# Kernel optimization log

Hardware: AMD Instinct MI355X
Metric: run time of the kernel (lower is better)

Reference implementation:

```python
import jax, jax.numpy as jnp
import numpy as np

N_NODES = 100000
N_EDGES = 1600000
D_FEAT = 256
HID = 128
DEG_DIM = 128  # data.degree_exist_matrix.shape[1]


def setup_inputs() -> dict:
    key = jax.random.key(0)
    ks = jax.random.split(key, 12)
    s = lambda fan_in: 1.0 / np.sqrt(fan_in)
    x = jax.random.normal(ks[0], (N_NODES, D_FEAT), dtype=jnp.float32)
    edge_index = jax.random.randint(ks[1], (2, N_EDGES), 0, N_NODES, dtype=jnp.int32)
    return {
        "x": x,
        "edge_index": edge_index,
        # GCNConv 1 / 2 (PyG stores weight [in,out], bias [out])
        "W1": jax.random.uniform(ks[2], (D_FEAT, HID), jnp.float32, -s(D_FEAT), s(D_FEAT)),
        "b1": jnp.zeros((HID,), jnp.float32),
        "W2": jax.random.uniform(ks[3], (HID, HID), jnp.float32, -s(HID), s(HID)),
        "b2": jnp.zeros((HID,), jnp.float32),
        # down_sample Linear(D_FEAT, HID)
        "Wd": jax.random.uniform(ks[4], (D_FEAT, HID), jnp.float32, -s(D_FEAT), s(D_FEAT)),
        "bd": jax.random.uniform(ks[5], (HID,), jnp.float32, -s(D_FEAT), s(D_FEAT)),
        # linear2: Degree_layer(HID, 1) ~ Linear(HID, 1)
        "Wdeg": jax.random.uniform(ks[6], (HID, 1), jnp.float32, -s(HID), s(HID)),
        "bdeg": jax.random.uniform(ks[7], (1,), jnp.float32, -s(HID), s(HID)),
        # linear3: Linear(HID, DEG_DIM)
        "W3": jax.random.uniform(ks[8], (HID, DEG_DIM), jnp.float32, -s(HID), s(HID)),
        "b3": jax.random.uniform(ks[9], (DEG_DIM,), jnp.float32, -s(HID), s(HID)),
    }


def gcn_conv(x, W, b, src, dst, n):
    """PyG GCNConv: D^-1/2 (A+I) D^-1/2 X W + b (symmetric norm, self-loops)."""
    h = x @ W  # [N, out]
    deg = jax.ops.segment_sum(jnp.ones_like(dst, dtype=h.dtype), dst, num_segments=n) + 1.0
    dinv = jax.lax.rsqrt(deg)  # deg >= 1 from self loop
    coef = dinv[src] * dinv[dst]  # [E]
    msgs = h[src] * coef[:, None]  # [E, out] -- dominant gather
    agg = jax.ops.segment_sum(msgs, dst, num_segments=n)
    agg = agg + h * (dinv * dinv)[:, None]  # self-loop contribution
    return agg + b


def reference(x, edge_index, W1, b1, W2, b2, Wd, bd, Wdeg, bdeg, W3, b3):
    n = x.shape[0]
    src, dst = edge_index[0], edge_index[1]
    original_x = x @ Wd + bd
    h = gcn_conv(x, W1, b1, src, dst, n)
    h = jax.nn.relu(h)  # dropout is identity in eval mode
    h = gcn_conv(h, W2, b2, src, dst, n)
    h = h + original_x  # residual
    result1 = jax.nn.log_softmax(h, axis=-1)        # [N, HID]
    result2 = (h @ Wdeg + bdeg).squeeze(-1)          # [N]
    result3 = h @ W3 + b3                            # [N, DEG_DIM]
    return (result1, result2, result3)
```

## Files before the change

### kernel.cpp

```cpp
#include <hip/hip_runtime.h>


typedef __attribute__((ext_vector_type(8))) short bf16x8;
typedef __attribute__((ext_vector_type(4))) float f32x4;

#define CDIV(a, b) (((a) + (b) - 1) / (b))

#define GLOBAL_AS __attribute__((address_space(1)))
#define LDS_AS __attribute__((address_space(3)))

__device__ __forceinline__ void gload16(const void* g, void* l) {
  __builtin_amdgcn_global_load_lds((const GLOBAL_AS unsigned int*)g,
                                   (LDS_AS unsigned int*)l, 16, 0, 0);
}

__device__ __forceinline__ float b2f(unsigned short u) {
  union { unsigned int i; float f; } x; x.i = ((unsigned int)u) << 16; return x.f;
}
__device__ __forceinline__ unsigned short f2b(float f) {
  union { float f; unsigned int i; } x; x.f = f;
  unsigned int r = x.i + 0x7fffu + ((x.i >> 16) & 1u);
  return (unsigned short)(r >> 16);
}
__device__ __forceinline__ void add2(float& a0, float& a1, unsigned int u) {
  union { unsigned int i; float f; } lo, hi;
  lo.i = u << 16; hi.i = u & 0xffff0000u;
  a0 += lo.f; a1 += hi.f;
}
__device__ __forceinline__ unsigned int pack2(float lo, float hi) {
  return __builtin_amdgcn_perm(__float_as_uint(hi) + 0x8000u,
                               __float_as_uint(lo) + 0x8000u, 0x07060302u);
}


__global__ void k_wtrans4(const float* __restrict__ W1, const float* __restrict__ Wd,
                          const float* __restrict__ W2, const float* __restrict__ W3,
                          unsigned short* __restrict__ W1t, unsigned short* __restrict__ Wdt,
                          unsigned short* __restrict__ W2t, unsigned short* __restrict__ W3t) {
  int idx = blockIdx.x * blockDim.x + threadIdx.x;
  const float* in; unsigned short* out; int K, N;
  if (idx < 32768)       { in = W1; out = W1t; K = 256; N = 128; }
  else if (idx < 65536)  { in = Wd; out = Wdt; K = 256; N = 128; idx -= 32768; }
  else if (idx < 81920)  { in = W2; out = W2t; K = 128; N = 128; idx -= 65536; }
  else if (idx < 98304)  { in = W3; out = W3t; K = 128; N = 128; idx -= 81920; }
  else return;
  int k = idx / N, n = idx - k * N;
  out[n * K + k] = f2b(in[idx]);
}

__global__ void k_scan1(const int* __restrict__ deg, int* __restrict__ lscan,
                        int* __restrict__ partials, float* __restrict__ dinv, int n) {
  __shared__ int sd[256];
  int tid = threadIdx.x;
  int base = blockIdx.x * 2048 + tid * 8;
  int v[8]; int tsum = 0;
#pragma unroll
  for (int i = 0; i < 8; ++i) {
    int idx = base + i;
    int xv = (idx < n) ? deg[idx] : 0;
    v[i] = xv; tsum += xv;
    if (idx < n) dinv[idx] = 1.0f / sqrtf((float)xv + 1.0f);
  }
  sd[tid] = tsum;
  __syncthreads();
  for (int off = 1; off < 256; off <<= 1) {
    int t = (tid >= off) ? sd[tid - off] : 0;
    __syncthreads();
    sd[tid] += t;
    __syncthreads();
  }
  int run = sd[tid] - tsum;
#pragma unroll
  for (int i = 0; i < 8; ++i) {
    int idx = base + i;
    if (idx < n) lscan[idx] = run;
    run += v[i];
  }
  if (tid == 255) partials[blockIdx.x] = sd[255];
}

__global__ void k_scan2(const int* __restrict__ partials, int* __restrict__ pprefix, int nb) {
  if (threadIdx.x == 0 && blockIdx.x == 0) {
    int run = 0;
    for (int i = 0; i < nb; ++i) { pprefix[i] = run; run += partials[i]; }
    pprefix[nb] = run;
  }
}

__global__ void k_scan3(const int* __restrict__ pprefix, int* row_start,
                        int* __restrict__ cursor, int n, int E) {
  int idx = blockIdx.x * blockDim.x + threadIdx.x;
  if (idx >= n) return;
  int v = row_start[idx] + pprefix[idx >> 11];
  row_start[idx] = v;
  cursor[idx] = v;
  if (idx == 0) row_start[n] = E;
}


#define BIN_CHUNK 4096
#define OVF_CAP 65536

__global__ __launch_bounds__(256) void k_binA(
    const int* __restrict__ ei, int E, int nbuck, int cap,
    int* __restrict__ deg, int2* __restrict__ pairs, int* __restrict__ bcnt,
    int2* __restrict__ ovf, int* __restrict__ ovf_cnt) {
  __shared__ int lcnt[256];
  __shared__ int lbase[256];
  int tid = threadIdx.x;
  for (int i = tid; i < nbuck; i += 256) lcnt[i] = 0;
  __syncthreads();
  int base_e = blockIdx.x * BIN_CHUNK;
  int src[16], dst[16], lofs[16];
#pragma unroll
  for (int i = 0; i < 16; ++i) {
    int e = base_e + i * 256 + tid;
    if (e < E) {
      int s = ei[e], d = ei[E + e];
      src[i] = s; dst[i] = d;
      atomicAdd(&deg[d], 1);
      lofs[i] = atomicAdd(&lcnt[d >> 9], 1);
    } else {
      dst[i] = -1;
    }
  }
  __syncthreads();
  for (int b = tid; b < nbuck; b += 256)
    lbase[b] = atomicAdd(&bcnt[b], lcnt[b]);
  __syncthreads();
#pragma unroll
  for (int i = 0; i < 16; ++i) {
    if (dst[i] < 0) continue;
    int b = dst[i] >> 9;
    int gpos = lbase[b] + lofs[i];
    if (gpos < cap) {
      pairs[(size_t)b * cap + gpos] = make_int2(src[i], dst[i]);
    } else {
      int op = atomicAdd(ovf_cnt, 1);
      if (op < OVF_CAP) ovf[op] = make_int2(src[i], dst[i]);
    }
  }
}

__global__ __launch_bounds__(256) void k_binB(
    const int2* __restrict__ pairs, const int* __restrict__ bcnt,
    int nbuck, int cap,
    const int2* __restrict__ ovf, const int* __restrict__ ovf_cnt,
    int* __restrict__ cursor, int* __restrict__ csr_src) {
  if ((int)blockIdx.x < nbuck) {
    int b = blockIdx.x;
    int cnt = bcnt[b]; if (cnt > cap) cnt = cap;
    const int2* p = pairs + (size_t)b * cap;
    for (int i = threadIdx.x; i < cnt; i += 256) {
      int2 e = p[i];
      int pos = atomicAdd(&cursor[e.y], 1);
      csr_src[pos] = e.x;
    }
  } else {
    int total = *ovf_cnt; if (total > OVF_CAP) total = OVF_CAP;
    int start = (blockIdx.x - nbuck) * 256 + threadIdx.x;
    for (int i = start; i < total; i += 8 * 256) {
      int2 e = ovf[i];
      int pos = atomicAdd(&cursor[e.y], 1);
      csr_src[pos] = e.x;
    }
  }
}


__global__ __launch_bounds__(512) void k_gemm_x2(
    const float* __restrict__ X,
    const unsigned short* __restrict__ B1t,
    const unsigned short* __restrict__ B2t,
    const float* __restrict__ bias2,
    const float* __restrict__ dinvp,
    unsigned short* __restrict__ O1, float* __restrict__ O2, int n) {
  __shared__ char lds[65536];
  const int flat = threadIdx.x;
  const int wave = flat >> 6, lane = flat & 63;
  const int l15 = lane & 15, q = lane >> 4;
  const int wM = wave >> 1, wN = wave & 1;
  const int rowBase = blockIdx.x * 128;
  const int colBase = wN * 64;

  auto stage = [&](int kb, int buf) {
    char* ldsA = lds + buf * 32768;
    char* ldsB = ldsA + 16384;
    const char* Xb = (const char*)X;
#pragma unroll
    for (int j = 0; j < 2; ++j) {
      int i = j * 512 + flat;
      int row = i >> 3, pslot = i & 7;
      int lslot = pslot ^ (row & 7);
      int rowc = rowBase + row; if (rowc >= n) rowc = n - 1;
      gload16(Xb + (size_t)rowc * 1024 + (size_t)(kb * 128 + lslot * 16),
              ldsA + (j * 512 + wave * 64) * 16);
    }
#pragma unroll
    for (int j = 0; j < 2; ++j) {
      int i = j * 512 + flat;
      int col = i >> 3, pslot = i & 7;
      int lslot = pslot ^ (col & 7);
      const char* src = (lslot >= 4) ? (const char*)B2t : (const char*)B1t;
      gload16(src + (size_t)col * 512 + kb * 64 + (lslot & 3) * 16,
              ldsB + (j * 512 + wave * 64) * 16);
    }
  };

  f32x4 acc1[2][4], acc2[2][4];
#pragma unroll
  for (int i = 0; i < 2; ++i)
#pragma unroll
    for (int j = 0; j < 4; ++j) {
      acc1[i][j] = (f32x4){0.f, 0.f, 0.f, 0.f};
      acc2[i][j] = (f32x4){0.f, 0.f, 0.f, 0.f};
    }

  stage(0, 0);
  __syncthreads();

#pragma unroll
  for (int kb = 0; kb < 8; ++kb) {
    int cur = kb & 1;
    if (kb < 7) stage(kb + 1, cur ^ 1);
    char* ldsA = lds + cur * 32768;
    char* ldsB = ldsA + 16384;
    bf16x8 a[2], b1v[4], b2v[4];
#pragma unroll
    for (int mt = 0; mt < 2; ++mt) {
      int row = wM * 32 + mt * 16 + l15;
      uint4 lo = *(const uint4*)(ldsA + row * 128 + (((2 * q) ^ (row & 7)) * 16));
      uint4 hi = *(const uint4*)(ldsA + row * 128 + (((2 * q + 1) ^ (row & 7)) * 16));
      union { bf16x8 v; unsigned int u[4]; } r;
      r.u[0] = __builtin_amdgcn_perm(lo.y + 0x8000u, lo.x + 0x8000u, 0x07060302u);
      r.u[1] = __builtin_amdgcn_perm(lo.w + 0x8000u, lo.z + 0x8000u, 0x07060302u);
      r.u[2] = __builtin_amdgcn_perm(hi.y + 0x8000u, hi.x + 0x8000u, 0x07060302u);
      r.u[3] = __builtin_amdgcn_perm(hi.w + 0x8000u, hi.z + 0x8000u, 0x07060302u);
      a[mt] = r.v;
    }
#pragma unroll
    for (int nt = 0; nt < 4; ++nt) {
      int col = colBase + nt * 16 + l15;
      b1v[nt] = *(const bf16x8*)(ldsB + col * 128 + ((q ^ (col & 7)) * 16));
      b2v[nt] = *(const bf16x8*)(ldsB + col * 128 + (((4 + q) ^ (col & 7)) * 16));
    }
#pragma unroll
    for (int mt = 0; mt < 2; ++mt)
#pragma unroll
      for (int nt = 0; nt < 4; ++nt) {
        acc1[mt][nt] = __builtin_amdgcn_mfma_f32_16x16x32_bf16(a[mt], b1v[nt], acc1[mt][nt], 0, 0, 0);
        acc2[mt][nt] = __builtin_amdgcn_mfma_f32_16x16x32_bf16(a[mt], b2v[nt], acc2[mt][nt], 0, 0, 0);
      }
    __syncthreads();
  }

#pragma unroll
  for (int mt = 0; mt < 2; ++mt) {
    float4 dv = *(const float4*)(dinvp + rowBase + wM * 32 + mt * 16 + q * 4);
#pragma unroll
    for (int nt = 0; nt < 4; ++nt) {
      int col = colBase + nt * 16 + l15;
      float bb = bias2[col];
#pragma unroll
      for (int r = 0; r < 4; ++r) {
        int row = rowBase + wM * 32 + mt * 16 + q * 4 + r;
        if (row < n) {
          float dvr = (r == 0) ? dv.x : (r == 1) ? dv.y : (r == 2) ? dv.z : dv.w;
          O1[(size_t)row * 128 + col] = f2b(acc1[mt][nt][r] * dvr);
          O2[(size_t)row * 128 + col] = acc2[mt][nt][r] + bb;
        }
      }
    }
  }
}

template <int OUT_F32>
__global__ __launch_bounds__(512) void k_gemm_h(
    const unsigned short* __restrict__ X, const unsigned short* __restrict__ Bt,
    const float* __restrict__ bias, const float* __restrict__ dinvp,
    unsigned short* __restrict__ Ob, float* __restrict__ Of, int n) {
  __shared__ char lds[65536];
  const int flat = threadIdx.x;
  const int wave = flat >> 6, lane = flat & 63;
  const int l15 = lane & 15, q = lane >> 4;
  const int wM = wave >> 1, wN = wave & 1;
  const int rowBase = blockIdx.x * 128;
  const int colBase = wN * 64;

  auto stage = [&](int ks, int buf) {
    char* ldsA = lds + buf * 32768;
    char* ldsB = ldsA + 16384;
#pragma unroll
    for (int j = 0; j < 2; ++j) {
      int i = j * 512 + flat;
      int row = i >> 3, pslot = i & 7;
      int lslot = pslot ^ (row & 7);
      int rowc = rowBase + row; if (rowc >= n) rowc = n - 1;
      gload16((const char*)X + (size_t)rowc * 256 + ks * 128 + lslot * 16,
              ldsA + (j * 512 + wave * 64) * 16);
    }
#pragma unroll
    for (int j = 0; j < 2; ++j) {
      int i = j * 512 + flat;
      int col = i >> 3, pslot = i & 7;
      int lslot = pslot ^ (col & 7);
      gload16((const char*)Bt + (size_t)col * 256 + ks * 128 + lslot * 16,
              ldsB + (j * 512 + wave * 64) * 16);
    }
  };

  f32x4 acc[2][4];
#pragma unroll
  for (int i = 0; i < 2; ++i)
#pragma unroll
    for (int j = 0; j < 4; ++j) acc[i][j] = (f32x4){0.f, 0.f, 0.f, 0.f};

  stage(0, 0);
  __syncthreads();
  stage(1, 1);

#pragma unroll
  for (int ks = 0; ks < 2; ++ks) {
    char* ldsA = lds + ks * 32768;
    char* ldsB = ldsA + 16384;
#pragma unroll
    for (int k2 = 0; k2 < 2; ++k2) {
      bf16x8 a[2], b[4];
#pragma unroll
      for (int mt = 0; mt < 2; ++mt) {
        int row = wM * 32 + mt * 16 + l15;
        a[mt] = *(const bf16x8*)(ldsA + row * 128 + (((k2 * 4 + q) ^ (row & 7)) * 16));
      }
#pragma unroll
      for (int nt = 0; nt < 4; ++nt) {
        int col = colBase + nt * 16 + l15;
        b[nt] = *(const bf16x8*)(ldsB + col * 128 + (((k2 * 4 + q) ^ (col & 7)) * 16));
      }
#pragma unroll
      for (int mt = 0; mt < 2; ++mt)
#pragma unroll
        for (int nt = 0; nt < 4; ++nt)
          acc[mt][nt] = __builtin_amdgcn_mfma_f32_16x16x32_bf16(a[mt], b[nt], acc[mt][nt], 0, 0, 0);
    }
    if (ks == 0) __syncthreads();
  }

#pragma unroll
  for (int mt = 0; mt < 2; ++mt) {
    float4 dv;
    if (!OUT_F32) dv = *(const float4*)(dinvp + rowBase + wM * 32 + mt * 16 + q * 4);
#pragma unroll
    for (int nt = 0; nt < 4; ++nt) {
      int col = colBase + nt * 16 + l15;
      float bb = OUT_F32 ? bias[col] : 0.f;
#pragma unroll
      for (int r = 0; r < 4; ++r) {
        int row = rowBase + wM * 32 + mt * 16 + q * 4 + r;
        if (row < n) {
          if (OUT_F32) {
            __builtin_nontemporal_store(acc[mt][nt][r] + bb, &Of[(size_t)row * 128 + col]);
          } else {
            float dvr = (r == 0) ? dv.x : (r == 1) ? dv.y : (r == 2) ? dv.z : dv.w;
            Ob[(size_t)row * 128 + col] = f2b(acc[mt][nt][r] * dvr);
          }
        }
      }
    }
  }
}


__device__ __forceinline__ void agg_edges4(
    const unsigned short* __restrict__ h, const int* __restrict__ csr_src,
    int beg, int end, int lane, int grp, int sub, float* acc) {
  for (int base = beg; base < end; base += 64) {
    int m = end - base; if (m > 64) m = 64;
    int idx_l = (base + lane < end) ? csr_src[base + lane] : 0;
    for (int j = 0; j < m; j += 16) {
      int s0 = __builtin_amdgcn_ds_bpermute((j + grp) << 2, idx_l);
      int s1 = __builtin_amdgcn_ds_bpermute((j + 4 + grp) << 2, idx_l);
      int s2 = __builtin_amdgcn_ds_bpermute((j + 8 + grp) << 2, idx_l);
      int s3 = __builtin_amdgcn_ds_bpermute((j + 12 + grp) << 2, idx_l);
      uint4 v0 = *(const uint4*)(h + (size_t)s0 * 128 + sub * 8);
      uint4 v1 = *(const uint4*)(h + (size_t)s1 * 128 + sub * 8);
      uint4 v2 = *(const uint4*)(h + (size_t)s2 * 128 + sub * 8);
      uint4 v3 = *(const uint4*)(h + (size_t)s3 * 128 + sub * 8);
      if (j + grp < m) {
        add2(acc[0], acc[1], v0.x); add2(acc[2], acc[3], v0.y);
        add2(acc[4], acc[5], v0.z); add2(acc[6], acc[7], v0.w);
      }
      if (j + 4 + grp < m) {
        add2(acc[0], acc[1], v1.x); add2(acc[2], acc[3], v1.y);
        add2(acc[4], acc[5], v1.z); add2(acc[6], acc[7], v1.w);
      }
      if (j + 8 + grp < m) {
        add2(acc[0], acc[1], v2.x); add2(acc[2], acc[3], v2.y);
        add2(acc[4], acc[5], v2.z); add2(acc[6], acc[7], v2.w);
      }
      if (j + 12 + grp < m) {
        add2(acc[0], acc[1], v3.x); add2(acc[2], acc[3], v3.y);
        add2(acc[4], acc[5], v3.z); add2(acc[6], acc[7], v3.w);
      }
    }
  }
}

__device__ __forceinline__ void grp_reduce(float* acc) {
#pragma unroll
  for (int i = 0; i < 8; ++i) {
    acc[i] += __shfl_xor(acc[i], 16);
    acc[i] += __shfl_xor(acc[i], 32);
  }
}

__global__ __launch_bounds__(256) void k_agg1(
    const unsigned short* __restrict__ h,
    const int* __restrict__ row_start, const int* __restrict__ csr_src,
    const float* __restrict__ dinv,
    const float* __restrict__ bias,
    unsigned short* __restrict__ hout, int n) {
  int gw = blockIdx.x * 4 + (threadIdx.x >> 6);
  int lane = threadIdx.x & 63;
  int grp = lane >> 4, sub = lane & 15;
  if (gw >= n) return;
  int beg = row_start[gw], end = row_start[gw + 1];
  float acc[8] = {0.f, 0.f, 0.f, 0.f, 0.f, 0.f, 0.f, 0.f};
  agg_edges4(h, csr_src, beg, end, lane, grp, sub, acc);
  grp_reduce(acc);
  if (grp == 0) {
    float dg = dinv[gw];
    uint4 sv = *(const uint4*)(h + (size_t)gw * 128 + sub * 8);
    add2(acc[0], acc[1], sv.x); add2(acc[2], acc[3], sv.y);
    add2(acc[4], acc[5], sv.z); add2(acc[6], acc[7], sv.w);
    float4 b0 = *(const float4*)(bias + sub * 8);
    float4 b1v = *(const float4*)(bias + sub * 8 + 4);
    float a[8];
    a[0] = fmaxf(acc[0] * dg + b0.x, 0.f); a[1] = fmaxf(acc[1] * dg + b0.y, 0.f);
    a[2] = fmaxf(acc[2] * dg + b0.z, 0.f); a[3] = fmaxf(acc[3] * dg + b0.w, 0.f);
    a[4] = fmaxf(acc[4] * dg + b1v.x, 0.f); a[5] = fmaxf(acc[5] * dg + b1v.y, 0.f);
    a[6] = fmaxf(acc[6] * dg + b1v.z, 0.f); a[7] = fmaxf(acc[7] * dg + b1v.w, 0.f);
    uint4 o;
    o.x = pack2(a[0], a[1]); o.y = pack2(a[2], a[3]);
    o.z = pack2(a[4], a[5]); o.w = pack2(a[6], a[7]);
    *(uint4*)(hout + (size_t)gw * 128 + sub * 8) = o;
  }
}

__global__ __launch_bounds__(256) void k_agg2_epi(
    const unsigned short* __restrict__ h,
    const int* __restrict__ row_start, const int* __restrict__ csr_src,
    const float* __restrict__ dinv,
    const float* __restrict__ bias,
    float* res_out1,
    const float* __restrict__ wdeg, const float* __restrict__ bdeg,
    float* __restrict__ out2,
    unsigned short* __restrict__ hf,
    int n) {
  int gw = blockIdx.x * 4 + (threadIdx.x >> 6);
  int lane = threadIdx.x & 63;
  int grp = lane >> 4, sub = lane & 15;
  if (gw >= n) return;
  int beg = row_start[gw], end = row_start[gw + 1];
  float acc[8] = {0.f, 0.f, 0.f, 0.f, 0.f, 0.f, 0.f, 0.f};
  agg_edges4(h, csr_src, beg, end, lane, grp, sub, acc);
  grp_reduce(acc);
  if (grp == 0) {
    float dg = dinv[gw];
    uint4 sv = *(const uint4*)(h + (size_t)gw * 128 + sub * 8);
    add2(acc[0], acc[1], sv.x); add2(acc[2], acc[3], sv.y);
    add2(acc[4], acc[5], sv.z); add2(acc[6], acc[7], sv.w);
    float4 b0 = *(const float4*)(bias + sub * 8);
    float4 b1v = *(const float4*)(bias + sub * 8 + 4);
    float4 r0 = *(const float4*)(res_out1 + (size_t)gw * 128 + sub * 8);
    float4 r1 = *(const float4*)(res_out1 + (size_t)gw * 128 + sub * 8 + 4);
    float a[8];
    a[0] = acc[0] * dg + b0.x + r0.x; a[1] = acc[1] * dg + b0.y + r0.y;
    a[2] = acc[2] * dg + b0.z + r0.z; a[3] = acc[3] * dg + b0.w + r0.w;
    a[4] = acc[4] * dg + b1v.x + r1.x; a[5] = acc[5] * dg + b1v.y + r1.y;
    a[6] = acc[6] * dg + b1v.z + r1.z; a[7] = acc[7] * dg + b1v.w + r1.w;
    uint4 o;
    o.x = pack2(a[0], a[1]); o.y = pack2(a[2], a[3]);
    o.z = pack2(a[4], a[5]); o.w = pack2(a[6], a[7]);
    *(uint4*)(hf + (size_t)gw * 128 + sub * 8) = o;
    float4 w0 = *(const float4*)(wdeg + sub * 8);
    float4 w1 = *(const float4*)(wdeg + sub * 8 + 4);
    float t = a[0] * w0.x + a[1] * w0.y + a[2] * w0.z + a[3] * w0.w +
              a[4] * w1.x + a[5] * w1.y + a[6] * w1.z + a[7] * w1.w;
#pragma unroll
    for (int mk = 8; mk >= 1; mk >>= 1) t += __shfl_xor(t, mk);
    if (sub == 0) __builtin_nontemporal_store(t + bdeg[0], out2 + gw);
    float mx = a[0];
#pragma unroll
    for (int i = 1; i < 8; ++i) mx = fmaxf(mx, a[i]);
#pragma unroll
    for (int mk = 8; mk >= 1; mk >>= 1) mx = fmaxf(mx, __shfl_xor(mx, mk));
    float l = 0.f;
#pragma unroll
    for (int i = 0; i < 8; ++i) l += __expf(a[i] - mx);
#pragma unroll
    for (int mk = 8; mk >= 1; mk >>= 1) l += __shfl_xor(l, mk);
    float ls = mx + __logf(l);
    f32x4 o0 = {a[0] - ls, a[1] - ls, a[2] - ls, a[3] - ls};
    f32x4 o1 = {a[4] - ls, a[5] - ls, a[6] - ls, a[7] - ls};
    __builtin_nontemporal_store(o0, (f32x4*)(res_out1 + (size_t)gw * 128 + sub * 8));
    __builtin_nontemporal_store(o1, (f32x4*)(res_out1 + (size_t)gw * 128 + sub * 8 + 4));
  }
}


extern "C" void kernel_launch(void* const* d_in, const int* in_sizes, int n_in,
                              void* d_out, int out_size, void* d_ws, size_t ws_size,
                              hipStream_t stream) {
  const float* x   = (const float*)d_in[0];
  const int*   ei  = (const int*)d_in[1];
  const float* W1  = (const float*)d_in[2];
  const float* b1  = (const float*)d_in[3];
  const float* W2  = (const float*)d_in[4];
  const float* b2  = (const float*)d_in[5];
  const float* Wd  = (const float*)d_in[6];
  const float* bd  = (const float*)d_in[7];
  const float* Wdg = (const float*)d_in[8];
  const float* bdg = (const float*)d_in[9];
  const float* W3  = (const float*)d_in[10];
  const float* b3  = (const float*)d_in[11];

  const int N = in_sizes[0] / 256;
  const int E = in_sizes[1] / 2;

  char* w = (char*)d_ws;
  auto alloc = [&](size_t bytes) {
    char* p = w;
    w += (bytes + 255) & ~(size_t)255;
    return p;
  };
  unsigned short* W1t  = (unsigned short*)alloc((size_t)256 * 128 * 2);
  unsigned short* Wdt  = (unsigned short*)alloc((size_t)256 * 128 * 2);
  unsigned short* W2t  = (unsigned short*)alloc((size_t)128 * 128 * 2);
  unsigned short* W3t  = (unsigned short*)alloc((size_t)128 * 128 * 2);
  unsigned short* bufC = (unsigned short*)alloc((size_t)N * 128 * 2);
  int*   deg      = (int*)alloc((size_t)N * 4);
  float* dinv     = (float*)alloc((size_t)(N + 128) * 4);
  int*   row_start= (int*)alloc((size_t)(N + 1) * 4);
  int*   cursor   = (int*)alloc((size_t)N * 4);
  int*   partials = (int*)alloc(4096);
  int*   pprefix  = (int*)alloc(4096);
  int*   csr_src  = (int*)alloc((size_t)E * 4);
  int*   bcnt     = (int*)alloc(2048);
  int*   ovf_cnt  = bcnt + 256;
  int2*  ovf      = (int2*)alloc((size_t)OVF_CAP * 8);

  float* out1 = (float*)d_out;
  float* out2 = out1 + (size_t)N * 128;
  float* out3 = out2 + (size_t)N;
  unsigned short* bufA = (unsigned short*)out3;

  const int nbuck = CDIV(N, 512);
  int cap = (E / nbuck) + (E / nbuck) / 2;
  cap = (cap + 255) & ~255;
  size_t bufC_bytes = (size_t)N * 128 * 2;
  if ((size_t)nbuck * cap * 8 > bufC_bytes)
    cap = (int)(bufC_bytes / ((size_t)nbuck * 8));
  int2* pairs = (int2*)bufC;

  hipMemsetAsync(deg, 0, (size_t)N * 4, stream);
  hipMemsetAsync(bcnt, 0, 2048, stream);

  k_wtrans4<<<CDIV(98304, 256), 256, 0, stream>>>(W1, Wd, W2, W3, W1t, Wdt, W2t, W3t);

  k_binA<<<CDIV(E, BIN_CHUNK), 256, 0, stream>>>(ei, E, nbuck, cap, deg, pairs,
                                                 bcnt, ovf, ovf_cnt);

  const int nb = CDIV(N, 2048);
  k_scan1<<<nb, 256, 0, stream>>>(deg, row_start, partials, dinv, N);
  k_scan2<<<1, 64, 0, stream>>>(partials, pprefix, nb);
  k_scan3<<<CDIV(N, 256), 256, 0, stream>>>(pprefix, row_start, cursor, N, E);

  k_gemm_x2<<<CDIV(N, 128), 512, 0, stream>>>(x, W1t, Wdt, bd, dinv, bufA, out1, N);

  k_binB<<<nbuck + 8, 256, 0, stream>>>(pairs, bcnt, nbuck, cap, ovf, ovf_cnt,
                                        cursor, csr_src);

  k_agg1<<<CDIV(N, 4), 256, 0, stream>>>(bufA, row_start, csr_src, dinv, b1, bufC, N);

  k_gemm_h<0><<<CDIV(N, 128), 512, 0, stream>>>(bufC, W2t, nullptr, dinv, bufA, nullptr, N);

  k_agg2_epi<<<CDIV(N, 4), 256, 0, stream>>>(bufA, row_start, csr_src, dinv,
                                             b2, out1, Wdg, bdg, out2, bufC, N);

  k_gemm_h<1><<<CDIV(N, 128), 512, 0, stream>>>(bufC, W3t, b3, nullptr, nullptr, out3, N);
}
```

Baseline: 533.0 us.

## Keep GEMM weights resident in LDS and stream A operands directly to registers

The x-GEMM becomes a persistent kernel with 256 blocks. Each block loads the full W1 and Wd bf16 weights into 128KB of LDS once, then loops over row tiles. The A operand is loaded straight from global memory into registers with a two-deep prefetch instead of being staged through LDS. The h-GEMMs likewise preload the whole weight matrix into LDS and read A directly into registers, which removes the per-k-step barriers and the A staging. The costs are uncoalesced per-lane global reads of A and higher LDS use that limits occupancy.

```diff
diff --git a/kernel.cpp b/kernel.cpp
--- a/kernel.cpp
+++ b/kernel.cpp
@@ -30,6 +30,14 @@
 __device__ __forceinline__ unsigned int pack2(float lo, float hi) {
   return __builtin_amdgcn_perm(__float_as_uint(hi) + 0x8000u,
                                __float_as_uint(lo) + 0x8000u, 0x07060302u);
+}
+__device__ __forceinline__ bf16x8 cvt8(uint4 lo, uint4 hi) {
+  union { bf16x8 v; unsigned int u[4]; } r;
+  r.u[0] = __builtin_amdgcn_perm(lo.y + 0x8000u, lo.x + 0x8000u, 0x07060302u);
+  r.u[1] = __builtin_amdgcn_perm(lo.w + 0x8000u, lo.z + 0x8000u, 0x07060302u);
+  r.u[2] = __builtin_amdgcn_perm(hi.y + 0x8000u, hi.x + 0x8000u, 0x07060302u);
+  r.u[3] = __builtin_amdgcn_perm(hi.w + 0x8000u, hi.z + 0x8000u, 0x07060302u);
+  return r.v;
 }
 
 
@@ -174,100 +182,99 @@
     const unsigned short* __restrict__ B2t,
     const float* __restrict__ bias2,
     const float* __restrict__ dinvp,
-    unsigned short* __restrict__ O1, float* __restrict__ O2, int n) {
-  __shared__ char lds[65536];
+    unsigned short* __restrict__ O1, float* __restrict__ O2, int n, int ntile) {
+  __shared__ char lds[131072];
   const int flat = threadIdx.x;
   const int wave = flat >> 6, lane = flat & 63;
   const int l15 = lane & 15, q = lane >> 4;
   const int wM = wave >> 1, wN = wave & 1;
-  const int rowBase = blockIdx.x * 128;
   const int colBase = wN * 64;
 
-  auto stage = [&](int kb, int buf) {
-    char* ldsA = lds + buf * 32768;
-    char* ldsB = ldsA + 16384;
-    const char* Xb = (const char*)X;
-#pragma unroll
-    for (int j = 0; j < 2; ++j) {
-      int i = j * 512 + flat;
-      int row = i >> 3, pslot = i & 7;
-      int lslot = pslot ^ (row & 7);
-      int rowc = rowBase + row; if (rowc >= n) rowc = n - 1;
-      gload16(Xb + (size_t)rowc * 1024 + (size_t)(kb * 128 + lslot * 16),
-              ldsA + (j * 512 + wave * 64) * 16);
-    }
-#pragma unroll
-    for (int j = 0; j < 2; ++j) {
-      int i = j * 512 + flat;
-      int col = i >> 3, pslot = i & 7;
-      int lslot = pslot ^ (col & 7);
-      const char* src = (lslot >= 4) ? (const char*)B2t : (const char*)B1t;
-      gload16(src + (size_t)col * 512 + kb * 64 + (lslot & 3) * 16,
-              ldsB + (j * 512 + wave * 64) * 16);
-    }
-  };
-
-  f32x4 acc1[2][4], acc2[2][4];
-#pragma unroll
-  for (int i = 0; i < 2; ++i)
-#pragma unroll
-    for (int j = 0; j < 4; ++j) {
-      acc1[i][j] = (f32x4){0.f, 0.f, 0.f, 0.f};
-      acc2[i][j] = (f32x4){0.f, 0.f, 0.f, 0.f};
-    }
-
-  stage(0, 0);
+#pragma unroll
+  for (int j = 0; j < 16; ++j) {
+    int i = j * 512 + flat;
+    const char* srcM = (j < 8) ? (const char*)B1t : (const char*)B2t;
+    int ii = (j < 8) ? i : i - 4096;
+    int col = ii >> 5, slot = ii & 31;
+    int lslot = slot ^ (col & 7);
+    gload16(srcM + (size_t)col * 512 + lslot * 16,
+            lds + ((size_t)j * 512 + wave * 64) * 16);
+  }
   __syncthreads();
 
-#pragma unroll
-  for (int kb = 0; kb < 8; ++kb) {
-    int cur = kb & 1;
-    if (kb < 7) stage(kb + 1, cur ^ 1);
-    char* ldsA = lds + cur * 32768;
-    char* ldsB = ldsA + 16384;
-    bf16x8 a[2], b1v[4], b2v[4];
+  for (int t = blockIdx.x; t < ntile; t += gridDim.x) {
+    const int rowBase = t * 128 + wM * 32;
+    int rowIdx[2];
 #pragma unroll
     for (int mt = 0; mt < 2; ++mt) {
-      int row = wM * 32 + mt * 16 + l15;
-      uint4 lo = *(const uint4*)(ldsA + row * 128 + (((2 * q) ^ (row & 7)) * 16));
-      uint4 hi = *(const uint4*)(ldsA + row * 128 + (((2 * q + 1) ^ (row & 7)) * 16));
-      union { bf16x8 v; unsigned int u[4]; } r;
-      r.u[0] = __builtin_amdgcn_perm(lo.y + 0x8000u, lo.x + 0x8000u, 0x07060302u);
-      r.u[1] = __builtin_amdgcn_perm(lo.w + 0x8000u, lo.z + 0x8000u, 0x07060302u);
-      r.u[2] = __builtin_amdgcn_perm(hi.y + 0x8000u, hi.x + 0x8000u, 0x07060302u);
-      r.u[3] = __builtin_amdgcn_perm(hi.w + 0x8000u, hi.z + 0x8000u, 0x07060302u);
-      a[mt] = r.v;
-    }
-#pragma unroll
-    for (int nt = 0; nt < 4; ++nt) {
-      int col = colBase + nt * 16 + l15;
-      b1v[nt] = *(const bf16x8*)(ldsB + col * 128 + ((q ^ (col & 7)) * 16));
-      b2v[nt] = *(const bf16x8*)(ldsB + col * 128 + (((4 + q) ^ (col & 7)) * 16));
-    }
-#pragma unroll
-    for (int mt = 0; mt < 2; ++mt)
+      int r = rowBase + mt * 16 + l15;
+      rowIdx[mt] = (r < n) ? r : (n - 1);
+    }
+    const char* pA0 = (const char*)X + (size_t)rowIdx[0] * 1024 + q * 32;
+    const char* pA1 = (const char*)X + (size_t)rowIdx[1] * 1024 + q * 32;
+
+    f32x4 acc1[2][4], acc2[2][4];
+#pragma unroll
+    for (int i = 0; i < 2; ++i)
+#pragma unroll
+      for (int j = 0; j < 4; ++j) {
+        acc1[i][j] = (f32x4){0.f, 0.f, 0.f, 0.f};
+        acc2[i][j] = (f32x4){0.f, 0.f, 0.f, 0.f};
+      }
+
+    uint4 buf[2][4];
+#pragma unroll
+    for (int p = 0; p < 2; ++p) {
+      buf[p][0] = *(const uint4*)(pA0 + p * 128);
+      buf[p][1] = *(const uint4*)(pA0 + p * 128 + 16);
+      buf[p][2] = *(const uint4*)(pA1 + p * 128);
+      buf[p][3] = *(const uint4*)(pA1 + p * 128 + 16);
+    }
+
+#pragma unroll
+    for (int kb = 0; kb < 8; ++kb) {
+      const int pp = kb & 1;
+      bf16x8 a[2];
+      a[0] = cvt8(buf[pp][0], buf[pp][1]);
+      a[1] = cvt8(buf[pp][2], buf[pp][3]);
+      if (kb < 6) {
+        buf[pp][0] = *(const uint4*)(pA0 + (kb + 2) * 128);
+        buf[pp][1] = *(const uint4*)(pA0 + (kb + 2) * 128 + 16);
+        buf[pp][2] = *(const uint4*)(pA1 + (kb + 2) * 128);
+        buf[pp][3] = *(const uint4*)(pA1 + (kb + 2) * 128 + 16);
+      }
+      bf16x8 b1v[4], b2v[4];
 #pragma unroll
       for (int nt = 0; nt < 4; ++nt) {
-        acc1[mt][nt] = __builtin_amdgcn_mfma_f32_16x16x32_bf16(a[mt], b1v[nt], acc1[mt][nt], 0, 0, 0);
-        acc2[mt][nt] = __builtin_amdgcn_mfma_f32_16x16x32_bf16(a[mt], b2v[nt], acc2[mt][nt], 0, 0, 0);
-      }
-    __syncthreads();
-  }
-
-#pragma unroll
-  for (int mt = 0; mt < 2; ++mt) {
-    float4 dv = *(const float4*)(dinvp + rowBase + wM * 32 + mt * 16 + q * 4);
-#pragma unroll
-    for (int nt = 0; nt < 4; ++nt) {
-      int col = colBase + nt * 16 + l15;
-      float bb = bias2[col];
-#pragma unroll
-      for (int r = 0; r < 4; ++r) {
-        int row = rowBase + wM * 32 + mt * 16 + q * 4 + r;
-        if (row < n) {
-          float dvr = (r == 0) ? dv.x : (r == 1) ? dv.y : (r == 2) ? dv.z : dv.w;
-          O1[(size_t)row * 128 + col] = f2b(acc1[mt][nt][r] * dvr);
-          O2[(size_t)row * 128 + col] = acc2[mt][nt][r] + bb;
+        int col = colBase + nt * 16 + l15;
+        int s = (kb * 4 + q) ^ (col & 7);
+        b1v[nt] = *(const bf16x8*)(lds + (size_t)col * 512 + s * 16);
+        b2v[nt] = *(const bf16x8*)(lds + 65536 + (size_t)col * 512 + s * 16);
+      }
+#pragma unroll
+      for (int mt = 0; mt < 2; ++mt)
+#pragma unroll
+        for (int nt = 0; nt < 4; ++nt) {
+          acc1[mt][nt] = __builtin_amdgcn_mfma_f32_16x16x32_bf16(a[mt], b1v[nt], acc1[mt][nt], 0, 0, 0);
+          acc2[mt][nt] = __builtin_amdgcn_mfma_f32_16x16x32_bf16(a[mt], b2v[nt], acc2[mt][nt], 0, 0, 0);
+        }
+    }
+
+#pragma unroll
+    for (int mt = 0; mt < 2; ++mt) {
+      float4 dv = *(const float4*)(dinvp + t * 128 + wM * 32 + mt * 16 + q * 4);
+#pragma unroll
+      for (int nt = 0; nt < 4; ++nt) {
+        int col = colBase + nt * 16 + l15;
+        float bb = bias2[col];
+#pragma unroll
+        for (int r = 0; r < 4; ++r) {
+          int row = t * 128 + wM * 32 + mt * 16 + q * 4 + r;
+          if (row < n) {
+            float dvr = (r == 0) ? dv.x : (r == 1) ? dv.y : (r == 2) ? dv.z : dv.w;
+            O1[(size_t)row * 128 + col] = f2b(acc1[mt][nt][r] * dvr);
+            O2[(size_t)row * 128 + col] = acc2[mt][nt][r] + bb;
+          }
         }
       }
     }
@@ -279,35 +286,39 @@
     const unsigned short* __restrict__ X, const unsigned short* __restrict__ Bt,
     const float* __restrict__ bias, const float* __restrict__ dinvp,
     unsigned short* __restrict__ Ob, float* __restrict__ Of, int n) {
-  __shared__ char lds[65536];
+  __shared__ char lds[32768];
   const int flat = threadIdx.x;
   const int wave = flat >> 6, lane = flat & 63;
   const int l15 = lane & 15, q = lane >> 4;
   const int wM = wave >> 1, wN = wave & 1;
-  const int rowBase = blockIdx.x * 128;
+  const int rowBase = blockIdx.x * 128 + wM * 32;
   const int colBase = wN * 64;
 
-  auto stage = [&](int ks, int buf) {
-    char* ldsA = lds + buf * 32768;
-    char* ldsB = ldsA + 16384;
-#pragma unroll
-    for (int j = 0; j < 2; ++j) {
-      int i = j * 512 + flat;
-      int row = i >> 3, pslot = i & 7;
-      int lslot = pslot ^ (row & 7);
-      int rowc = rowBase + row; if (rowc >= n) rowc = n - 1;
-      gload16((const char*)X + (size_t)rowc * 256 + ks * 128 + lslot * 16,
-              ldsA + (j * 512 + wave * 64) * 16);
-    }
-#pragma unroll
-    for (int j = 0; j < 2; ++j) {
-      int i = j * 512 + flat;
-      int col = i >> 3, pslot = i & 7;
-      int lslot = pslot ^ (col & 7);
-      gload16((const char*)Bt + (size_t)col * 256 + ks * 128 + lslot * 16,
-              ldsB + (j * 512 + wave * 64) * 16);
-    }
-  };
+  int rowIdx[2];
+#pragma unroll
+  for (int mt = 0; mt < 2; ++mt) {
+    int r = rowBase + mt * 16 + l15;
+    rowIdx[mt] = (r < n) ? r : (n - 1);
+  }
+  const char* pA0 = (const char*)X + (size_t)rowIdx[0] * 256 + q * 16;
+  const char* pA1 = (const char*)X + (size_t)rowIdx[1] * 256 + q * 16;
+
+  uint4 buf[2][2];
+#pragma unroll
+  for (int p = 0; p < 2; ++p) {
+    buf[p][0] = *(const uint4*)(pA0 + p * 64);
+    buf[p][1] = *(const uint4*)(pA1 + p * 64);
+  }
+
+#pragma unroll
+  for (int j = 0; j < 4; ++j) {
+    int i = j * 512 + flat;
+    int col = i >> 4, slot = i & 15;
+    int lslot = slot ^ (col & 7);
+    gload16((const char*)Bt + (size_t)col * 256 + lslot * 16,
+            lds + ((size_t)j * 512 + wave * 64) * 16);
+  }
+  __syncthreads();
 
   f32x4 acc[2][4];
 #pragma unroll
@@ -315,47 +326,41 @@
 #pragma unroll
     for (int j = 0; j < 4; ++j) acc[i][j] = (f32x4){0.f, 0.f, 0.f, 0.f};
 
-  stage(0, 0);
-  __syncthreads();
-  stage(1, 1);
-
-#pragma unroll
-  for (int ks = 0; ks < 2; ++ks) {
-    char* ldsA = lds + ks * 32768;
-    char* ldsB = ldsA + 16384;
-#pragma unroll
-    for (int k2 = 0; k2 < 2; ++k2) {
-      bf16x8 a[2], b[4];
-#pragma unroll
-      for (int mt = 0; mt < 2; ++mt) {
-        int row = wM * 32 + mt * 16 + l15;
-        a[mt] = *(const bf16x8*)(ldsA + row * 128 + (((k2 * 4 + q) ^ (row & 7)) * 16));
-      }
-#pragma unroll
-      for (int nt = 0; nt < 4; ++nt) {
-        int col = colBase + nt * 16 + l15;
-        b[nt] = *(const bf16x8*)(ldsB + col * 128 + (((k2 * 4 + q) ^ (col & 7)) * 16));
-      }
-#pragma unroll
-      for (int mt = 0; mt < 2; ++mt)
-#pragma unroll
-        for (int nt = 0; nt < 4; ++nt)
-          acc[mt][nt] = __builtin_amdgcn_mfma_f32_16x16x32_bf16(a[mt], b[nt], acc[mt][nt], 0, 0, 0);
-    }
-    if (ks == 0) __syncthreads();
+#pragma unroll
+  for (int kb = 0; kb < 4; ++kb) {
+    const int pp = kb & 1;
+    bf16x8 a[2];
+    a[0] = *(const bf16x8*)&buf[pp][0];
+    a[1] = *(const bf16x8*)&buf[pp][1];
+    if (kb < 2) {
+      buf[pp][0] = *(const uint4*)(pA0 + (kb + 2) * 64);
+      buf[pp][1] = *(const uint4*)(pA1 + (kb + 2) * 64);
+    }
+    bf16x8 b[4];
+#pragma unroll
+    for (int nt = 0; nt < 4; ++nt) {
+      int col = colBase + nt * 16 + l15;
+      int s = (kb * 4 + q) ^ (col & 7);
+      b[nt] = *(const bf16x8*)(lds + (size_t)col * 256 + s * 16);
+    }
+#pragma unroll
+    for (int mt = 0; mt < 2; ++mt)
+#pragma unroll
+      for (int nt = 0; nt < 4; ++nt)
+        acc[mt][nt] = __builtin_amdgcn_mfma_f32_16x16x32_bf16(a[mt], b[nt], acc[mt][nt], 0, 0, 0);
   }
 
 #pragma unroll
   for (int mt = 0; mt < 2; ++mt) {
     float4 dv;
-    if (!OUT_F32) dv = *(const float4*)(dinvp + rowBase + wM * 32 + mt * 16 + q * 4);
+    if (!OUT_F32) dv = *(const float4*)(dinvp + rowBase + mt * 16 + q * 4);
 #pragma unroll
     for (int nt = 0; nt < 4; ++nt) {
       int col = colBase + nt * 16 + l15;
       float bb = OUT_F32 ? bias[col] : 0.f;
 #pragma unroll
       for (int r = 0; r < 4; ++r) {
-        int row = rowBase + wM * 32 + mt * 16 + q * 4 + r;
+        int row = rowBase + mt * 16 + q * 4 + r;
         if (row < n) {
           if (OUT_F32) {
             __builtin_nontemporal_store(acc[mt][nt][r] + bb, &Of[(size_t)row * 128 + col]);
@@ -575,7 +580,8 @@
   k_scan2<<<1, 64, 0, stream>>>(partials, pprefix, nb);
   k_scan3<<<CDIV(N, 256), 256, 0, stream>>>(pprefix, row_start, cursor, N, E);
 
-  k_gemm_x2<<<CDIV(N, 128), 512, 0, stream>>>(x, W1t, Wdt, bd, dinv, bufA, out1, N);
+  k_gemm_x2<<<256, 512, 0, stream>>>(x, W1t, Wdt, bd, dinv, bufA, out1, N,
+                                     CDIV(N, 128));
 
   k_binB<<<nbuck + 8, 256, 0, stream>>>(pairs, bcnt, nbuck, cap, ovf, ovf_cnt,
                                         cursor, csr_src);
```

Result: slower. 625.7 us (+17.4%).
